# Optimization experiments

Measured on AMD Instinct MI355X. Metric: run time of the kernel, lower is better.

The kernel has to match this reference:

```python
import jax, jax.numpy as jnp
import numpy as np

B, F, D, DENSE, CARD = 16384, 26, 64, 13, 100000
H_BOT, H_TOP = 8, 16  # hardcoded hidden sizes in the torch module


def setup_inputs() -> dict:
    key = jax.random.key(0)
    ks = jax.random.split(key, 12)
    dense_x = jax.random.normal(ks[0], (B, DENSE), dtype=jnp.float32)
    sparse_x = jax.random.randint(ks[1], (B, F), 0, CARD, dtype=jnp.int64)
    # all tables share cardinality -> stack into one [F, CARD, D] tensor
    tables = jax.random.normal(ks[2], (F, CARD, D), dtype=jnp.float32) * 0.01
    # bottom MLP: dense_dim -> 8 -> embedding_dim
    w1 = jax.random.normal(ks[3], (DENSE, H_BOT), dtype=jnp.float32) * (1.0 / np.sqrt(DENSE))
    b1 = jnp.zeros((H_BOT,), dtype=jnp.float32)
    w2 = jax.random.normal(ks[4], (H_BOT, D), dtype=jnp.float32) * (1.0 / np.sqrt(H_BOT))
    b2 = jnp.zeros((D,), dtype=jnp.float32)
    # top MLP: F*D + D -> 16 -> 1, sigmoid
    top_in = F * D + D
    tw1 = jax.random.normal(ks[5], (top_in, H_TOP), dtype=jnp.float32) * (1.0 / np.sqrt(top_in))
    tb1 = jnp.zeros((H_TOP,), dtype=jnp.float32)
    tw2 = jax.random.normal(ks[6], (H_TOP, 1), dtype=jnp.float32) * (1.0 / np.sqrt(H_TOP))
    tb2 = jnp.zeros((1,), dtype=jnp.float32)
    return {"dense_x": dense_x, "sparse_x": sparse_x, "tables": tables,
            "w1": w1, "b1": b1, "w2": w2, "b2": b2,
            "tw1": tw1, "tb1": tb1, "tw2": tw2, "tb2": tb2}


def reference(dense_x, sparse_x, tables, w1, b1, w2, b2, tw1, tb1, tw2, tb2):
    # bottom MLP
    dense_out = jnp.maximum(dense_x @ w1 + b1, 0.0) @ w2 + b2  # [B, D]
    # per-table gather, vectorized over the F tables
    emb = jax.vmap(lambda t, idx: t[idx], in_axes=(0, 1), out_axes=1)(tables, sparse_x)  # [B, F, D]
    interaction = jnp.concatenate([emb.reshape(emb.shape[0], -1), dense_out], axis=1)  # [B, F*D + D]
    # top MLP
    logits = jnp.maximum(interaction @ tw1 + tb1, 0.0) @ tw2 + tb2  # [B, 1]
    return jax.nn.sigmoid(logits)
```

## Files before the change

### kernel.cpp

```cpp
#include <hip/hip_runtime.h>
#include <hip/hip_bf16.h>
#include <cmath>

typedef __bf16 bf16_t;
typedef bf16_t bf16x8 __attribute__((ext_vector_type(8)));
typedef float floatx4 __attribute__((ext_vector_type(4)));

#define NFEAT 26
#define DIM 64
#define DENSE_IN 13
#define CARD 100000
#define HBOT 8
#define KSTEPS 54

__global__ __launch_bounds__(256, 1) void dlrm_fused(
    const float* __restrict__ dense_x,
    const int* __restrict__ sparse_x,
    const float* __restrict__ tables,
    const float* __restrict__ w1, const float* __restrict__ b1,
    const float* __restrict__ w2, const float* __restrict__ b2,
    const float* __restrict__ tw1, const float* __restrict__ tb1,
    const float* __restrict__ tw2, const float* __restrict__ tb2,
    float* __restrict__ out)
{
    __shared__ __align__(16) bf16_t Blds[KSTEPS * 64 * 8];
    __shared__ __align__(16) bf16_t Dlds[4 * 2 * 64 * 8];
    __shared__ int idx_lds[64 * NFEAT];

    const int tid   = threadIdx.x;
    const int block = blockIdx.x;
    const int lane  = tid & 63;
    const int wave  = tid >> 6;

    const int* sp = sparse_x + (long)block * 64 * NFEAT;
    for (int i = tid; i < 64 * NFEAT; i += 256) idx_lds[i] = sp[i];

    for (int slot = tid; slot < KSTEPS * 64; slot += 256) {
        int t  = slot >> 6;
        int l  = slot & 63;
        int n  = l & 15;
        int k0 = t * 32 + (l >> 4) * 8;
        bf16x8 v;
        #pragma unroll
        for (int j = 0; j < 8; ++j)
            v[j] = (bf16_t)tw1[(k0 + j) * 16 + n];
        *(bf16x8*)(&Blds[slot * 8]) = v;
    }

    for (int slot = tid; slot < 512; slot += 256) {
        int tile = slot >> 7;
        int tp   = (slot >> 6) & 1;
        int l    = slot & 63;
        int m    = l & 15;
        int q    = l >> 4;
        int s    = block * 64 + tile * 16 + m;
        int d0   = tp * 32 + q * 8;
        float x[DENSE_IN];
        #pragma unroll
        for (int i = 0; i < DENSE_IN; ++i) x[i] = dense_x[s * DENSE_IN + i];
        float h8[HBOT];
        #pragma unroll
        for (int j = 0; j < HBOT; ++j) {
            float acc = b1[j];
            #pragma unroll
            for (int i = 0; i < DENSE_IN; ++i) acc = fmaf(x[i], w1[i * HBOT + j], acc);
            h8[j] = fmaxf(acc, 0.f);
        }
        bf16x8 v;
        #pragma unroll
        for (int jj = 0; jj < 8; ++jj) {
            float acc = b2[d0 + jj];
            #pragma unroll
            for (int j = 0; j < HBOT; ++j) acc = fmaf(h8[j], w2[j * DIM + d0 + jj], acc);
            v[jj] = (bf16_t)acc;
        }
        *(bf16x8*)(&Dlds[slot * 8]) = v;
    }

    __syncthreads();

    const int tile = wave;
    const int m    = lane & 15;
    const int q    = lane >> 4;
    floatx4 acc = {0.f, 0.f, 0.f, 0.f};

    const int* myidx = &idx_lds[(tile * 16 + m) * NFEAT];

    #pragma unroll 2
    for (int f = 0; f < NFEAT; ++f) {
        int idx = myidx[f];
        const float* row = tables + (long)(f * CARD + idx) * DIM;
        #pragma unroll
        for (int h = 0; h < 2; ++h) {
            const float4 p0 = *(const float4*)(row + h * 32 + q * 8);
            const float4 p1 = *(const float4*)(row + h * 32 + q * 8 + 4);
            bf16x8 a;
            a[0] = (bf16_t)p0.x; a[1] = (bf16_t)p0.y;
            a[2] = (bf16_t)p0.z; a[3] = (bf16_t)p0.w;
            a[4] = (bf16_t)p1.x; a[5] = (bf16_t)p1.y;
            a[6] = (bf16_t)p1.z; a[7] = (bf16_t)p1.w;
            bf16x8 b = *(bf16x8*)(&Blds[((f * 2 + h) * 64 + lane) * 8]);
            acc = __builtin_amdgcn_mfma_f32_16x16x32_bf16(a, b, acc, 0, 0, 0);
        }
    }
    #pragma unroll
    for (int tp = 0; tp < 2; ++tp) {
        bf16x8 a = *(bf16x8*)(&Dlds[((tile * 2 + tp) * 64 + lane) * 8]);
        bf16x8 b = *(bf16x8*)(&Blds[((52 + tp) * 64 + lane) * 8]);
        acc = __builtin_amdgcn_mfma_f32_16x16x32_bf16(a, b, acc, 0, 0, 0);
    }

    const int h = lane & 15;
    const float bias = tb1[h];
    const float wout = tw2[h];
    float p[4];
    #pragma unroll
    for (int i = 0; i < 4; ++i) p[i] = fmaxf(acc[i] + bias, 0.f) * wout;
    #pragma unroll
    for (int off = 1; off < 16; off <<= 1) {
        #pragma unroll
        for (int i = 0; i < 4; ++i) p[i] += __shfl_xor(p[i], off, 64);
    }
    if (h == 0) {
        const float bout = tb2[0];
        #pragma unroll
        for (int i = 0; i < 4; ++i) {
            float logit = p[i] + bout;
            out[block * 64 + tile * 16 + q * 4 + i] = 1.f / (1.f + expf(-logit));
        }
    }
}

extern "C" void kernel_launch(void* const* d_in, const int* in_sizes, int n_in,
                              void* d_out, int out_size, void* d_ws, size_t ws_size,
                              hipStream_t stream) {
    const float* dense_x = (const float*)d_in[0];
    const int*   sparse_x = (const int*)d_in[1];
    const float* tables  = (const float*)d_in[2];
    const float* w1  = (const float*)d_in[3];
    const float* b1  = (const float*)d_in[4];
    const float* w2  = (const float*)d_in[5];
    const float* b2  = (const float*)d_in[6];
    const float* tw1 = (const float*)d_in[7];
    const float* tb1 = (const float*)d_in[8];
    const float* tw2 = (const float*)d_in[9];
    const float* tb2 = (const float*)d_in[10];
    float* out = (float*)d_out;

    dlrm_fused<<<256, 256, 0, stream>>>(dense_x, sparse_x, tables,
                                        w1, b1, w2, b2,
                                        tw1, tb1, tw2, tb2, out);
}
```

Measured before the change: 747.6 us.

## Split prep into separate kernels and split feature loop across waves

Moves the tw1 bf16 repacking and the bottom MLP out of the main kernel into two small prep kernels that write to workspace. The main kernel then runs 512 blocks of 32 samples, and each sample's 26 features are split across two waves whose partial MFMA accumulators are combined through shared memory. The aim is more gather parallelism and memory-level concurrency, and no longer redoing the weight repack in every block. In exchange it adds two extra launches, workspace traffic, and B-operand reads from global memory instead of LDS.

```diff
diff --git a/kernel.cpp b/kernel.cpp
--- a/kernel.cpp
+++ b/kernel.cpp
@@ -13,83 +13,88 @@
 #define HBOT 8
 #define KSTEPS 54
 
-__global__ __launch_bounds__(256, 1) void dlrm_fused(
+
+__global__ __launch_bounds__(256) void prep_b(const float* __restrict__ tw1,
+                                              bf16_t* __restrict__ ws_b) {
+    int slot = blockIdx.x * 256 + threadIdx.x;
+    if (slot >= KSTEPS * 64) return;
+    int t  = slot >> 6;
+    int l  = slot & 63;
+    int n  = l & 15;
+    int k0 = t * 32 + (l >> 4) * 8;
+    bf16x8 v;
+    #pragma unroll
+    for (int j = 0; j < 8; ++j)
+        v[j] = (bf16_t)tw1[(k0 + j) * 16 + n];
+    *(bf16x8*)(ws_b + slot * 8) = v;
+}
+
+__global__ __launch_bounds__(256) void prep_dense(
     const float* __restrict__ dense_x,
-    const int* __restrict__ sparse_x,
-    const float* __restrict__ tables,
     const float* __restrict__ w1, const float* __restrict__ b1,
     const float* __restrict__ w2, const float* __restrict__ b2,
-    const float* __restrict__ tw1, const float* __restrict__ tb1,
-    const float* __restrict__ tw2, const float* __restrict__ tb2,
-    float* __restrict__ out)
-{
-    __shared__ __align__(16) bf16_t Blds[KSTEPS * 64 * 8];
-    __shared__ __align__(16) bf16_t Dlds[4 * 2 * 64 * 8];
-    __shared__ int idx_lds[64 * NFEAT];
-
-    const int tid   = threadIdx.x;
-    const int block = blockIdx.x;
-    const int lane  = tid & 63;
-    const int wave  = tid >> 6;
-
-    const int* sp = sparse_x + (long)block * 64 * NFEAT;
-    for (int i = tid; i < 64 * NFEAT; i += 256) idx_lds[i] = sp[i];
-
-    for (int slot = tid; slot < KSTEPS * 64; slot += 256) {
-        int t  = slot >> 6;
-        int l  = slot & 63;
-        int n  = l & 15;
-        int k0 = t * 32 + (l >> 4) * 8;
-        bf16x8 v;
+    bf16_t* __restrict__ ws_d) {
+    int s = blockIdx.x * 256 + threadIdx.x;
+    float x[DENSE_IN];
+    #pragma unroll
+    for (int i = 0; i < DENSE_IN; ++i) x[i] = dense_x[s * DENSE_IN + i];
+    float h8[HBOT];
+    #pragma unroll
+    for (int j = 0; j < HBOT; ++j) {
+        float acc = b1[j];
         #pragma unroll
-        for (int j = 0; j < 8; ++j)
-            v[j] = (bf16_t)tw1[(k0 + j) * 16 + n];
-        *(bf16x8*)(&Blds[slot * 8]) = v;
+        for (int i = 0; i < DENSE_IN; ++i) acc = fmaf(x[i], w1[i * HBOT + j], acc);
+        h8[j] = fmaxf(acc, 0.f);
     }
-
-    for (int slot = tid; slot < 512; slot += 256) {
-        int tile = slot >> 7;
-        int tp   = (slot >> 6) & 1;
-        int l    = slot & 63;
-        int m    = l & 15;
-        int q    = l >> 4;
-        int s    = block * 64 + tile * 16 + m;
-        int d0   = tp * 32 + q * 8;
-        float x[DENSE_IN];
-        #pragma unroll
-        for (int i = 0; i < DENSE_IN; ++i) x[i] = dense_x[s * DENSE_IN + i];
-        float h8[HBOT];
-        #pragma unroll
-        for (int j = 0; j < HBOT; ++j) {
-            float acc = b1[j];
-            #pragma unroll
-            for (int i = 0; i < DENSE_IN; ++i) acc = fmaf(x[i], w1[i * HBOT + j], acc);
-            h8[j] = fmaxf(acc, 0.f);
-        }
+    #pragma unroll
+    for (int c = 0; c < 8; ++c) {
         bf16x8 v;
         #pragma unroll
         for (int jj = 0; jj < 8; ++jj) {
-            float acc = b2[d0 + jj];
+            int d = c * 8 + jj;
+            float acc = b2[d];
             #pragma unroll
-            for (int j = 0; j < HBOT; ++j) acc = fmaf(h8[j], w2[j * DIM + d0 + jj], acc);
+            for (int j = 0; j < HBOT; ++j) acc = fmaf(h8[j], w2[j * DIM + d], acc);
             v[jj] = (bf16_t)acc;
         }
-        *(bf16x8*)(&Dlds[slot * 8]) = v;
+        *(bf16x8*)(ws_d + s * DIM + c * 8) = v;
+    }
+}
+
+__global__ __launch_bounds__(256) void dlrm_main(
+    const int* __restrict__ sparse_x,
+    const float* __restrict__ tables,
+    const bf16_t* __restrict__ ws_b,
+    const bf16_t* __restrict__ ws_d,
+    const float* __restrict__ tb1,
+    const float* __restrict__ tw2,
+    const float* __restrict__ tb2,
+    float* __restrict__ out) {
+    __shared__ float partial[2][64][4];
+
+    const int block = blockIdx.x;
+    const int tid   = threadIdx.x;
+    const int lane  = tid & 63;
+    const int wave  = tid >> 6;
+    const int tile  = wave & 1;
+    const int half  = wave >> 1;
+    const int m     = lane & 15;
+    const int q     = lane >> 4;
+    const int sample = block * 32 + tile * 16 + m;
+
+    int idxs[13];
+    {
+        const int* myidx = sparse_x + sample * NFEAT + half * 13;
+        #pragma unroll
+        for (int i = 0; i < 13; ++i) idxs[i] = myidx[i];
     }
 
-    __syncthreads();
-
-    const int tile = wave;
-    const int m    = lane & 15;
-    const int q    = lane >> 4;
     floatx4 acc = {0.f, 0.f, 0.f, 0.f};
 
-    const int* myidx = &idx_lds[(tile * 16 + m) * NFEAT];
-
-    #pragma unroll 2
-    for (int f = 0; f < NFEAT; ++f) {
-        int idx = myidx[f];
-        const float* row = tables + (long)(f * CARD + idx) * DIM;
+    #pragma unroll 4
+    for (int ff = 0; ff < 13; ++ff) {
+        const int f = half * 13 + ff;
+        const float* row = tables + ((long)f * CARD + idxs[ff]) * DIM;
         #pragma unroll
         for (int h = 0; h < 2; ++h) {
             const float4 p0 = *(const float4*)(row + h * 32 + q * 8);
@@ -99,34 +104,46 @@
             a[2] = (bf16_t)p0.z; a[3] = (bf16_t)p0.w;
             a[4] = (bf16_t)p1.x; a[5] = (bf16_t)p1.y;
             a[6] = (bf16_t)p1.z; a[7] = (bf16_t)p1.w;
-            bf16x8 b = *(bf16x8*)(&Blds[((f * 2 + h) * 64 + lane) * 8]);
+            bf16x8 b = *(const bf16x8*)(ws_b + ((f * 2 + h) * 64 + lane) * 8);
             acc = __builtin_amdgcn_mfma_f32_16x16x32_bf16(a, b, acc, 0, 0, 0);
         }
     }
-    #pragma unroll
-    for (int tp = 0; tp < 2; ++tp) {
-        bf16x8 a = *(bf16x8*)(&Dlds[((tile * 2 + tp) * 64 + lane) * 8]);
-        bf16x8 b = *(bf16x8*)(&Blds[((52 + tp) * 64 + lane) * 8]);
-        acc = __builtin_amdgcn_mfma_f32_16x16x32_bf16(a, b, acc, 0, 0, 0);
+
+    if (half == 0) {
+        #pragma unroll
+        for (int tp = 0; tp < 2; ++tp) {
+            bf16x8 a = *(const bf16x8*)(ws_d + sample * DIM + tp * 32 + q * 8);
+            bf16x8 b = *(const bf16x8*)(ws_b + ((52 + tp) * 64 + lane) * 8);
+            acc = __builtin_amdgcn_mfma_f32_16x16x32_bf16(a, b, acc, 0, 0, 0);
+        }
+    } else {
+        #pragma unroll
+        for (int i = 0; i < 4; ++i) partial[tile][lane][i] = acc[i];
     }
+    __syncthreads();
 
-    const int h = lane & 15;
-    const float bias = tb1[h];
-    const float wout = tw2[h];
-    float p[4];
-    #pragma unroll
-    for (int i = 0; i < 4; ++i) p[i] = fmaxf(acc[i] + bias, 0.f) * wout;
-    #pragma unroll
-    for (int off = 1; off < 16; off <<= 1) {
+    if (half == 0) {
         #pragma unroll
-        for (int i = 0; i < 4; ++i) p[i] += __shfl_xor(p[i], off, 64);
-    }
-    if (h == 0) {
-        const float bout = tb2[0];
+        for (int i = 0; i < 4; ++i) acc[i] += partial[tile][lane][i];
+
+        const int h = lane & 15;
+        const float bias = tb1[h];
+        const float wout = tw2[h];
+        float p[4];
         #pragma unroll
-        for (int i = 0; i < 4; ++i) {
-            float logit = p[i] + bout;
-            out[block * 64 + tile * 16 + q * 4 + i] = 1.f / (1.f + expf(-logit));
+        for (int i = 0; i < 4; ++i) p[i] = fmaxf(acc[i] + bias, 0.f) * wout;
+        #pragma unroll
+        for (int off = 1; off < 16; off <<= 1) {
+            #pragma unroll
+            for (int i = 0; i < 4; ++i) p[i] += __shfl_xor(p[i], off, 64);
+        }
+        if (h == 0) {
+            const float bout = tb2[0];
+            #pragma unroll
+            for (int i = 0; i < 4; ++i) {
+                float logit = p[i] + bout;
+                out[block * 32 + tile * 16 + q * 4 + i] = 1.f / (1.f + expf(-logit));
+            }
         }
     }
 }
@@ -134,9 +151,9 @@
 extern "C" void kernel_launch(void* const* d_in, const int* in_sizes, int n_in,
                               void* d_out, int out_size, void* d_ws, size_t ws_size,
                               hipStream_t stream) {
-    const float* dense_x = (const float*)d_in[0];
+    const float* dense_x  = (const float*)d_in[0];
     const int*   sparse_x = (const int*)d_in[1];
-    const float* tables  = (const float*)d_in[2];
+    const float* tables   = (const float*)d_in[2];
     const float* w1  = (const float*)d_in[3];
     const float* b1  = (const float*)d_in[4];
     const float* w2  = (const float*)d_in[5];
@@ -147,7 +164,11 @@
     const float* tb2 = (const float*)d_in[10];
     float* out = (float*)d_out;
 
-    dlrm_fused<<<256, 256, 0, stream>>>(dense_x, sparse_x, tables,
-                                        w1, b1, w2, b2,
-                                        tw1, tb1, tw2, tb2, out);
+    bf16_t* ws_b = (bf16_t*)d_ws;
+    bf16_t* ws_d = (bf16_t*)((char*)d_ws + 65536);
+
+    prep_b<<<(KSTEPS * 64 + 255) / 256, 256, 0, stream>>>(tw1, ws_b);
+    prep_dense<<<16384 / 256, 256, 0, stream>>>(dense_x, w1, b1, w2, b2, ws_d);
+    dlrm_main<<<512, 256, 0, stream>>>(sparse_x, tables, ws_b, ws_d,
+                                       tb1, tw2, tb2, out);
 }
```

Measured after the change: 749.4 us. Within noise of the previous version (+0.2%).
